# Kernel optimization log

Measured on AMD Instinct MI355X. Metric: run time of the kernel, lower is better.

Reference implementation:

```python
import jax, jax.numpy as jnp
import numpy as np

F = 32          # conf['num_features']
G = 96          # voxel grid extent
N_VOX = 80000   # occupied input voxels
BN_EPS = 1e-5


def _encode(c):
    c = c.astype(np.int64) + 8
    return (c[:, 0] * 512 + c[:, 1]) * 512 + c[:, 2]


def _offsets(ks, dil):
    r = np.arange(-(ks // 2), ks // 2 + 1) * dil
    return np.stack(np.meshgrid(r, r, r, indexing='ij'), -1).reshape(-1, 3)


def _build_map(in_coords, out_coords, offsets):
    # For each kernel offset k and output voxel j, find input voxel index at
    # out_coords[j] + offsets[k]; sentinel = n_in / n_out when absent.
    n_in, n_out = len(in_coords), len(out_coords)
    keys = _encode(in_coords)
    order = np.argsort(keys).astype(np.int32)
    skeys = keys[order]
    K = len(offsets)
    in_map = np.full((K, n_out), n_in, np.int32)
    out_map = np.full((K, n_out), n_out, np.int32)
    base = np.arange(n_out, dtype=np.int32)
    for k, off in enumerate(offsets):
        q = _encode(out_coords + off)
        pos = np.clip(np.searchsorted(skeys, q), 0, n_in - 1)
        valid = skeys[pos] == q
        in_map[k] = np.where(valid, order[pos], n_in)
        out_map[k] = np.where(valid, base, n_out)
    return jnp.asarray(in_map), jnp.asarray(out_map)


def setup_inputs() -> dict:
    rng = np.random.default_rng(0)
    idx = rng.choice(G ** 3, size=N_VOX, replace=False)
    coords = np.stack(np.unravel_index(idx, (G, G, G)), 1).astype(np.int64)
    c2 = np.unique(coords // 2 * 2, axis=0)   # stride-2 coords (enc1 output)
    c4 = np.unique(coords // 4 * 4, axis=0)   # stride-4 coords (c_out.C)

    m1_in, m1_out = _build_map(coords, c2, _offsets(5, 1))  # k5 s2 conv
    m2_in, m2_out = _build_map(c2, c2, _offsets(3, 2))      # enc1 blocks
    m3_in, m3_out = _build_map(c2, c4, _offsets(3, 2))      # conv2 -> c_out.C
    m4_in, m4_out = _build_map(c4, c4, _offsets(3, 4))      # enc2 blocks

    key = jax.random.key(0)
    ks = jax.random.split(key, 8)
    s = 0.05
    return {
        'x_geo': jax.random.normal(ks[0], (N_VOX, 1), jnp.float32),
        'x_col': jax.random.uniform(ks[1], (N_VOX, 3), jnp.float32),
        'w0': jax.random.normal(ks[2], (125, 4, F), jnp.float32) * s,
        'w_e1': jax.random.normal(ks[3], (2, 2, 27, F, F), jnp.float32) * s,
        'g_e1': jnp.ones((2, 2, F), jnp.float32),
        'b_e1': jnp.zeros((2, 2, F), jnp.float32),
        'w2': jax.random.normal(ks[4], (27, F, 2 * F), jnp.float32) * s,
        'w_e2': jax.random.normal(ks[5], (2, 2, 27, 2 * F, 2 * F), jnp.float32) * s,
        'g_e2': jnp.ones((2, 2, 2 * F), jnp.float32),
        'b_e2': jnp.zeros((2, 2, 2 * F), jnp.float32),
        'm1_in': m1_in, 'm1_out': m1_out,
        'm2_in': m2_in, 'm2_out': m2_out,
        'm3_in': m3_in, 'm3_out': m3_out,
        'm4_in': m4_in, 'm4_out': m4_out,
    }


def sparse_conv(feats, W, in_map, out_map):
    # gather -> GEMM -> scatter per kernel offset (lax.scan over K offsets)
    n_out = out_map.shape[1]
    fpad = jnp.concatenate([feats, jnp.zeros((1, feats.shape[1]), feats.dtype)], 0)
    out0 = jnp.zeros((n_out + 1, W.shape[2]), feats.dtype)
    def step(acc, kmw):
        im, om, w = kmw
        return acc.at[om].add(fpad[im] @ w), None
    out, _ = jax.lax.scan(step, out0, (in_map, out_map, W))
    return out[:n_out]


def batch_norm(x, g, b):
    mu = x.mean(0)
    var = ((x - mu) ** 2).mean(0)
    return (x - mu) * jax.lax.rsqrt(var + BN_EPS) * g + b


def basic_block(x, w, g, b, in_map, out_map):
    # ME BasicBlock: conv-BN-ReLU-conv-BN + residual, ReLU
    y = jax.nn.relu(batch_norm(sparse_conv(x, w[0], in_map, out_map), g[0], b[0]))
    y = batch_norm(sparse_conv(y, w[1], in_map, out_map), g[1], b[1])
    return jax.nn.relu(y + x)


def reference(x_geo, x_col, w0, w_e1, g_e1, b_e1, w2, w_e2, g_e2, b_e2,
              m1_in, m1_out, m2_in, m2_out, m3_in, m3_out, m4_in, m4_out):
    x = jnp.concatenate([x_geo, x_col], axis=1)          # ME.cat -> 4 channels
    x = jax.nn.relu(sparse_conv(x, w0, m1_in, m1_out))   # k5 s2 conv + ReLU
    for i in range(2):                                   # enc1 residual blocks
        x = basic_block(x, w_e1[i], g_e1[i], b_e1[i], m2_in, m2_out)
    x = sparse_conv(x, w2, m3_in, m3_out)                # conv2 onto c_out.C
    for i in range(2):                                   # enc2 residual blocks
        x = basic_block(x, w_e2[i], g_e2[i], b_e2[i], m4_in, m4_out)
    return x
```

## Files before the change

kernel.cpp:

```cpp
#include <hip/hip_runtime.h>
#include <hip/hip_bf16.h>


typedef float f4 __attribute__((ext_vector_type(4)));
typedef short short8 __attribute__((ext_vector_type(8)));
typedef short short4v __attribute__((ext_vector_type(4)));

#define BN_EPS 1e-5f

static inline int ceil_div(int a, int b) { return (a + b - 1) / b; }

static __device__ inline float btof(short s) {
    unsigned u = ((unsigned)(unsigned short)s) << 16;
    float f;
    __builtin_memcpy(&f, &u, 4);
    return f;
}
static __device__ inline short ftob(float f) {
    __hip_bfloat16 h = __float2bfloat16(f);
    short s;
    __builtin_memcpy(&s, &h, 2);
    return s;
}

struct Seg {
    const float* W;
    long long begin, end;
    int K, CIN, COUT;
};
struct ProArgs {
    Seg s[10];
    const float* geo;
    const float* col;
    __hip_bfloat16* x0;
    int n_vox;
    float* stats;
    __hip_bfloat16* pads[5];
    int padn[5];
    long long wf_total;
    __hip_bfloat16* Wf;
};

__global__ __launch_bounds__(256) void prologue(ProArgs pa, long long total) {
    long long e = (long long)blockIdx.x * 256 + threadIdx.x;
    if (e >= total) return;
    if (e < pa.wf_total) {
        int si = 0;
#pragma unroll
        for (int i = 0; i < 10; ++i)
            if (e >= pa.s[i].end) si = i + 1;
        const Seg sg = pa.s[si];
        long long r = e - sg.begin;
        int j = (int)(r & 7);
        int lane = (int)((r >> 3) & 63);
        long long rest = r >> 9;
        int NT = sg.COUT >> 4;
        int ntile = (int)(rest % NT);
        int chunk = (int)(rest / NT);
        int kd = chunk * 32 + ((lane >> 4) << 3) + j;
        int koff = kd / sg.CIN;
        int ci = kd % sg.CIN;
        int n = ntile * 16 + (lane & 15);
        float v = (koff < sg.K) ? sg.W[((size_t)koff * sg.CIN + ci) * sg.COUT + n] : 0.f;
        pa.Wf[e] = __float2bfloat16(v);
        return;
    }
    long long r = e - pa.wf_total;
    if (r < pa.n_vox) {
        int row = (int)r;
        pa.x0[row * 4 + 0] = __float2bfloat16(pa.geo[row]);
        pa.x0[row * 4 + 1] = __float2bfloat16(pa.col[row * 3 + 0]);
        pa.x0[row * 4 + 2] = __float2bfloat16(pa.col[row * 3 + 1]);
        pa.x0[row * 4 + 3] = __float2bfloat16(pa.col[row * 3 + 2]);
        return;
    }
    r -= pa.n_vox;
    if (r < 4096) {
        pa.stats[r] = 0.f;
        return;
    }
    r -= 4096;
#pragma unroll
    for (int i = 0; i < 5; ++i) {
        if (r < pa.padn[i]) {
            pa.pads[i][r] = __float2bfloat16(0.f);
            return;
        }
        r -= pa.padn[i];
    }
}

template <int CIN, int COUT, int MT, int K>
__global__ __launch_bounds__(256) void conv_splitk(
    const __hip_bfloat16* __restrict__ feat,
    const __hip_bfloat16* __restrict__ Wf,
    const int* __restrict__ in_map,
    __hip_bfloat16* __restrict__ out,
    float* __restrict__ stats,
    int n_out, int n_in) {
    constexpr int NT = COUT / 16;
    constexpr int H = CIN / 32;
    constexpr int R = MT * 16;
    constexpr int KPW = (K + 3) / 4;
    const int t = threadIdx.x, w = t >> 6, lane = t & 63;
    const int quad = lane >> 4, ml = lane & 15;
    const int mb = blockIdx.x * R;

    __shared__ float red[4][R][COUT];
    __shared__ float sred[2][256];

    f4 acc[MT * NT];
#pragma unroll
    for (int i = 0; i < MT * NT; ++i) acc[i] = (f4){0.f, 0.f, 0.f, 0.f};

    for (int kk = 0; kk < KPW; ++kk) {
        const int k = kk * 4 + w;
        if (k < K) {
            const int* mk = in_map + (size_t)k * n_out;
            int idx[MT];
#pragma unroll
            for (int mi = 0; mi < MT; ++mi) {
                int m = mb + mi * 16 + ml;
                idx[mi] = (m < n_out) ? mk[m] : n_in;
            }
            short8 bfrag[H * NT];
#pragma unroll
            for (int h = 0; h < H; ++h)
#pragma unroll
                for (int nt = 0; nt < NT; ++nt)
                    bfrag[h * NT + nt] = *(const short8*)(
                        Wf + (((size_t)(k * H + h) * NT + nt) * 64 + lane) * 8);
#pragma unroll
            for (int mi = 0; mi < MT; ++mi) {
                const __hip_bfloat16* fp = feat + (size_t)idx[mi] * CIN + quad * 8;
#pragma unroll
                for (int h = 0; h < H; ++h) {
                    short8 a = *(const short8*)(fp + h * 32);
#pragma unroll
                    for (int nt = 0; nt < NT; ++nt)
                        acc[mi * NT + nt] = __builtin_amdgcn_mfma_f32_16x16x32_bf16(
                            a, bfrag[h * NT + nt], acc[mi * NT + nt], 0, 0, 0);
                }
            }
        }
    }

#pragma unroll
    for (int mi = 0; mi < MT; ++mi)
#pragma unroll
        for (int nt = 0; nt < NT; ++nt)
#pragma unroll
            for (int i = 0; i < 4; ++i)
                red[w][mi * 16 + quad * 4 + i][nt * 16 + ml] = acc[mi * NT + nt][i];
    __syncthreads();

    constexpr int E = (R * COUT) / 256;
    constexpr int RSTEP = 256 / COUT;
    const int col = t % COUT;
    const int rg = t / COUT;
    float s = 0.f, s2 = 0.f;
#pragma unroll
    for (int i = 0; i < E; ++i) {
        int r = rg + i * RSTEP;
        float v = red[0][r][col] + red[1][r][col] + red[2][r][col] + red[3][r][col];
        s += v;
        s2 += v * v;
        int grow = mb + r;
        if (grow < n_out) out[(size_t)grow * COUT + col] = __float2bfloat16(v);
    }

    if (stats) {
        sred[0][t] = s;
        sred[1][t] = s2;
        __syncthreads();
        if (t < 2 * COUT) {
            int c = t % COUT;
            int which = t / COUT;
            float v = 0.f;
#pragma unroll
            for (int j = 0; j < RSTEP; ++j) v += sred[which][j * COUT + c];
            atomicAdd(&stats[((blockIdx.x & 3) * 2 + which) * COUT + c], v);
        }
    }
}

__global__ __launch_bounds__(256) void stem_mfma(
    const __hip_bfloat16* __restrict__ feat,
    const __hip_bfloat16* __restrict__ Wf,
    const int* __restrict__ in_map,
    __hip_bfloat16* __restrict__ out,
    int n_out, int n_in) {
    const int t = threadIdx.x, w = t >> 6, lane = t & 63;
    const int quad = lane >> 4, ml = lane & 15;
    const int ntile = w & 1, mgroup = w >> 1;
    const int mb = blockIdx.x * 64 + mgroup * 32;
    const int m0 = mb + ml, m1 = mb + 16 + ml;
    const bool v0 = m0 < n_out, v1 = m1 < n_out;

    f4 acc0 = {0.f, 0.f, 0.f, 0.f};
    f4 acc1 = {0.f, 0.f, 0.f, 0.f};

#pragma unroll 4
    for (int chunk = 0; chunk < 16; ++chunk) {
        int k0 = chunk * 8 + quad * 2;
        int k1 = k0 + 1;
        short8 b = *(const short8*)(Wf + ((size_t)(chunk * 2 + ntile) * 64 + lane) * 8);
        int ia = (v0 && k0 < 125) ? in_map[(size_t)k0 * n_out + m0] : n_in;
        int ib = (v0 && k1 < 125) ? in_map[(size_t)k1 * n_out + m0] : n_in;
        int ic = (v1 && k0 < 125) ? in_map[(size_t)k0 * n_out + m1] : n_in;
        int id = (v1 && k1 < 125) ? in_map[(size_t)k1 * n_out + m1] : n_in;
        short4v pa = *(const short4v*)(feat + (size_t)ia * 4);
        short4v pb = *(const short4v*)(feat + (size_t)ib * 4);
        short4v pc = *(const short4v*)(feat + (size_t)ic * 4);
        short4v pd = *(const short4v*)(feat + (size_t)id * 4);
        short8 a0, a1;
        a0[0] = pa[0]; a0[1] = pa[1]; a0[2] = pa[2]; a0[3] = pa[3];
        a0[4] = pb[0]; a0[5] = pb[1]; a0[6] = pb[2]; a0[7] = pb[3];
        a1[0] = pc[0]; a1[1] = pc[1]; a1[2] = pc[2]; a1[3] = pc[3];
        a1[4] = pd[0]; a1[5] = pd[1]; a1[6] = pd[2]; a1[7] = pd[3];
        acc0 = __builtin_amdgcn_mfma_f32_16x16x32_bf16(a0, b, acc0, 0, 0, 0);
        acc1 = __builtin_amdgcn_mfma_f32_16x16x32_bf16(a1, b, acc1, 0, 0, 0);
    }

    const int col = ntile * 16 + ml;
#pragma unroll
    for (int i = 0; i < 4; ++i) {
        int r0 = mb + quad * 4 + i;
        if (r0 < n_out)
            out[(size_t)r0 * 32 + col] = __float2bfloat16(fmaxf(acc0[i], 0.f));
        int r1 = mb + 16 + quad * 4 + i;
        if (r1 < n_out)
            out[(size_t)r1 * 32 + col] = __float2bfloat16(fmaxf(acc1[i], 0.f));
    }
}

template <int C>
__device__ inline void bn_coef(const float* st, const float* g, const float* b,
                               int c, int n, float& sc, float& sh) {
    float rn = 1.f / (float)n;
    float sum = st[c] + st[2 * C + c] + st[4 * C + c] + st[6 * C + c];
    float sq  = st[C + c] + st[3 * C + c] + st[5 * C + c] + st[7 * C + c];
    float mu = sum * rn;
    float inv = rsqrtf(sq * rn - mu * mu + BN_EPS);
    sc = inv * g[c];
    sh = b[c] - mu * sc;
}

template <int C>
__global__ __launch_bounds__(256) void bn_relu8(
    __hip_bfloat16* __restrict__ x, const float* __restrict__ st,
    const float* __restrict__ g, const float* __restrict__ b, int n) {
    __shared__ float sc[C], sh[C];
    const int t = threadIdx.x;
    if (t < C) bn_coef<C>(st, g, b, t, n, sc[t], sh[t]);
    __syncthreads();
    long long i = (long long)blockIdx.x * 256 + t;
    long long tot = (long long)n * (C / 8);
    if (i >= tot) return;
    int c0 = (int)(i % (C / 8)) * 8;
    short8 v = *(const short8*)(x + i * 8);
    short8 o;
#pragma unroll
    for (int j = 0; j < 8; ++j) {
        float f = btof(v[j]) * sc[c0 + j] + sh[c0 + j];
        o[j] = ftob(fmaxf(f, 0.f));
    }
    *(short8*)(x + i * 8) = o;
}

template <int C>
__global__ __launch_bounds__(256) void bn_res8_bf16(
    const __hip_bfloat16* __restrict__ y, const __hip_bfloat16* __restrict__ res,
    const float* __restrict__ st, const float* __restrict__ g,
    const float* __restrict__ b, __hip_bfloat16* __restrict__ out, int n) {
    __shared__ float sc[C], sh[C];
    const int t = threadIdx.x;
    if (t < C) bn_coef<C>(st, g, b, t, n, sc[t], sh[t]);
    __syncthreads();
    long long i = (long long)blockIdx.x * 256 + t;
    long long tot = (long long)n * (C / 8);
    if (i >= tot) return;
    int c0 = (int)(i % (C / 8)) * 8;
    short8 v = *(const short8*)(y + i * 8);
    short8 r = *(const short8*)(res + i * 8);
    short8 o;
#pragma unroll
    for (int j = 0; j < 8; ++j) {
        float f = btof(v[j]) * sc[c0 + j] + sh[c0 + j] + btof(r[j]);
        o[j] = ftob(fmaxf(f, 0.f));
    }
    *(short8*)(out + i * 8) = o;
}

template <int C>
__global__ __launch_bounds__(256) void bn_res8_f32(
    const __hip_bfloat16* __restrict__ y, const __hip_bfloat16* __restrict__ res,
    const float* __restrict__ st, const float* __restrict__ g,
    const float* __restrict__ b, float* __restrict__ out, int n) {
    __shared__ float sc[C], sh[C];
    const int t = threadIdx.x;
    if (t < C) bn_coef<C>(st, g, b, t, n, sc[t], sh[t]);
    __syncthreads();
    long long i = (long long)blockIdx.x * 256 + t;
    long long tot = (long long)n * (C / 8);
    if (i >= tot) return;
    int c0 = (int)(i % (C / 8)) * 8;
    short8 v = *(const short8*)(y + i * 8);
    short8 r = *(const short8*)(res + i * 8);
    f4 o0, o1;
#pragma unroll
    for (int j = 0; j < 8; ++j) {
        float f = btof(v[j]) * sc[c0 + j] + sh[c0 + j] + btof(r[j]);
        f = fmaxf(f, 0.f);
        if (j < 4) o0[j] = f; else o1[j - 4] = f;
    }
    *(f4*)(out + i * 8) = o0;
    *(f4*)(out + i * 8 + 4) = o1;
}

extern "C" void kernel_launch(void* const* d_in, const int* in_sizes, int n_in_cnt,
                              void* d_out, int out_size, void* d_ws, size_t ws_size,
                              hipStream_t stream) {
    const float* x_geo = (const float*)d_in[0];
    const float* x_col = (const float*)d_in[1];
    const float* w0    = (const float*)d_in[2];
    const float* w_e1  = (const float*)d_in[3];
    const float* g_e1  = (const float*)d_in[4];
    const float* b_e1  = (const float*)d_in[5];
    const float* w2    = (const float*)d_in[6];
    const float* w_e2  = (const float*)d_in[7];
    const float* g_e2  = (const float*)d_in[8];
    const float* b_e2  = (const float*)d_in[9];
    const int* m1_in = (const int*)d_in[10];
    const int* m2_in = (const int*)d_in[12];
    const int* m3_in = (const int*)d_in[14];
    const int* m4_in = (const int*)d_in[16];

    const int n_vox = in_sizes[0];
    const int nc2 = in_sizes[10] / 125;
    const int nc4 = in_sizes[14] / 27;
    (void)out_size; (void)ws_size; (void)n_in_cnt;

    char* p = (char*)d_ws;
    auto alloc = [&](size_t bytes) -> char* {
        char* r = p;
        p += (bytes + 255) & ~(size_t)255;
        return r;
    };
    float* stats = (float*)alloc(8 * 512 * sizeof(float));
    __hip_bfloat16* x0 = (__hip_bfloat16*)alloc((size_t)(n_vox + 1) * 4 * 2);
    __hip_bfloat16* A  = (__hip_bfloat16*)alloc((size_t)(nc2 + 1) * 32 * 2);
    __hip_bfloat16* B  = (__hip_bfloat16*)alloc((size_t)(nc2 + 1) * 32 * 2);
    __hip_bfloat16* Cb = (__hip_bfloat16*)alloc((size_t)(nc2 + 1) * 32 * 2);
    __hip_bfloat16* D  = (__hip_bfloat16*)alloc((size_t)(nc4 + 1) * 64 * 2);
    __hip_bfloat16* E  = (__hip_bfloat16*)alloc((size_t)(nc4 + 1) * 64 * 2);
    __hip_bfloat16* Fb = (__hip_bfloat16*)alloc((size_t)(nc4 + 1) * 64 * 2);

    const long long sz_stem = 16LL * 2 * 512;
    const long long sz_e1   = 27LL * 2 * 512;
    const long long sz_c2   = 27LL * 4 * 512;
    const long long sz_e2   = 54LL * 4 * 512;
    const long long wf_total = sz_stem + 4 * sz_e1 + sz_c2 + 4 * sz_e2;
    __hip_bfloat16* Wf = (__hip_bfloat16*)alloc((size_t)wf_total * 2);

    long long off_stem = 0;
    long long off_e1[4], off_e2[4];
    long long cur = sz_stem;
    for (int i = 0; i < 4; ++i) { off_e1[i] = cur; cur += sz_e1; }
    long long off_c2 = cur; cur += sz_c2;
    for (int i = 0; i < 4; ++i) { off_e2[i] = cur; cur += sz_e2; }

    ProArgs pa;
    cur = 0;
    auto seg = [&](int i, const float* W, int K, int CIN, int COUT, long long n) {
        pa.s[i].W = W; pa.s[i].K = K; pa.s[i].CIN = CIN; pa.s[i].COUT = COUT;
        pa.s[i].begin = cur; pa.s[i].end = cur + n; cur += n;
    };
    seg(0, w0, 125, 4, 32, sz_stem);
    for (int i = 0; i < 4; ++i)
        seg(1 + i, w_e1 + (size_t)i * 27 * 32 * 32, 27, 32, 32, sz_e1);
    seg(5, w2, 27, 32, 64, sz_c2);
    for (int i = 0; i < 4; ++i)
        seg(6 + i, w_e2 + (size_t)i * 27 * 64 * 64, 27, 64, 64, sz_e2);
    pa.geo = x_geo; pa.col = x_col; pa.x0 = x0; pa.n_vox = n_vox;
    pa.stats = stats;
    pa.pads[0] = x0 + (size_t)n_vox * 4; pa.padn[0] = 4;
    pa.pads[1] = A + (size_t)nc2 * 32;   pa.padn[1] = 32;
    pa.pads[2] = B + (size_t)nc2 * 32;   pa.padn[2] = 32;
    pa.pads[3] = D + (size_t)nc4 * 64;   pa.padn[3] = 64;
    pa.pads[4] = E + (size_t)nc4 * 64;   pa.padn[4] = 64;
    pa.wf_total = wf_total;
    pa.Wf = Wf;
    long long pro_total = wf_total + n_vox + 4096 + (4 + 32 + 32 + 64 + 64);
    prologue<<<ceil_div((int)pro_total, 256), 256, 0, stream>>>(pa, pro_total);

    stem_mfma<<<ceil_div(nc2, 64), 256, 0, stream>>>(x0, Wf + off_stem, m1_in, A,
                                                     nc2, n_vox);

    int slot = 0;
    for (int blk = 0; blk < 2; ++blk) {
        const float* gA = g_e1 + (blk * 2 + 0) * 32, *bA = b_e1 + (blk * 2 + 0) * 32;
        const float* gB = g_e1 + (blk * 2 + 1) * 32, *bB = b_e1 + (blk * 2 + 1) * 32;
        conv_splitk<32, 32, 2, 27><<<ceil_div(nc2, 32), 256, 0, stream>>>(
            A, Wf + off_e1[blk * 2 + 0], m2_in, B, stats + slot * 512, nc2, nc2);
        bn_relu8<32><<<ceil_div(nc2 * 4, 256), 256, 0, stream>>>(
            B, stats + slot * 512, gA, bA, nc2);
        ++slot;
        conv_splitk<32, 32, 2, 27><<<ceil_div(nc2, 32), 256, 0, stream>>>(
            B, Wf + off_e1[blk * 2 + 1], m2_in, Cb, stats + slot * 512, nc2, nc2);
        bn_res8_bf16<32><<<ceil_div(nc2 * 4, 256), 256, 0, stream>>>(
            Cb, A, stats + slot * 512, gB, bB, A, nc2);
        ++slot;
    }

    conv_splitk<32, 64, 1, 27><<<ceil_div(nc4, 16), 256, 0, stream>>>(
        A, Wf + off_c2, m3_in, D, nullptr, nc4, nc2);

    for (int blk = 0; blk < 2; ++blk) {
        const float* gA = g_e2 + (blk * 2 + 0) * 64, *bA = b_e2 + (blk * 2 + 0) * 64;
        const float* gB = g_e2 + (blk * 2 + 1) * 64, *bB = b_e2 + (blk * 2 + 1) * 64;
        conv_splitk<64, 64, 1, 27><<<ceil_div(nc4, 16), 256, 0, stream>>>(
            D, Wf + off_e2[blk * 2 + 0], m4_in, E, stats + slot * 512, nc4, nc4);
        bn_relu8<64><<<ceil_div(nc4 * 8, 256), 256, 0, stream>>>(
            E, stats + slot * 512, gA, bA, nc4);
        ++slot;
        conv_splitk<64, 64, 1, 27><<<ceil_div(nc4, 16), 256, 0, stream>>>(
            E, Wf + off_e2[blk * 2 + 1], m4_in, Fb, stats + slot * 512, nc4, nc4);
        if (blk == 0) {
            bn_res8_bf16<64><<<ceil_div(nc4 * 8, 256), 256, 0, stream>>>(
                Fb, D, stats + slot * 512, gB, bB, D, nc4);
        } else {
            bn_res8_f32<64><<<ceil_div(nc4 * 8, 256), 256, 0, stream>>>(
                Fb, D, stats + slot * 512, gB, bB, (float*)d_out, nc4);
        }
        ++slot;
    }
}
```

Before: 360.1 us.

## Fuse BN+ReLU of first block conv into second conv's gather

Drops the standalone bn_relu8 kernels. The second conv of each residual block now applies batch-norm scale/shift and ReLU to the gathered bf16 features as it loads them, masking sentinel rows to zero. The K loop is fully unrolled with a clamped map row, so out-of-range kernel offsets read weights from an extra zero-padded slot (weight buffers are sized up by one offset) instead of branching. This saves a launch and a full read/write pass per block. In exchange, the normalization arithmetic is repeated for every gathered neighbour (up to 27 times per voxel) and register pressure rises.

```diff
diff --git a/kernel.cpp b/kernel.cpp
--- a/kernel.cpp
+++ b/kernel.cpp
@@ -90,13 +90,28 @@
     }
 }
 
-template <int CIN, int COUT, int MT, int K>
+template <int C>
+__device__ inline void bn_coef(const float* st, const float* g, const float* b,
+                               int c, int n, float& sc, float& sh) {
+    float rn = 1.f / (float)n;
+    float sum = st[c] + st[2 * C + c] + st[4 * C + c] + st[6 * C + c];
+    float sq  = st[C + c] + st[3 * C + c] + st[5 * C + c] + st[7 * C + c];
+    float mu = sum * rn;
+    float inv = rsqrtf(sq * rn - mu * mu + BN_EPS);
+    sc = inv * g[c];
+    sh = b[c] - mu * sc;
+}
+
+template <int CIN, int COUT, int MT, int K, bool BNF>
 __global__ __launch_bounds__(256) void conv_splitk(
     const __hip_bfloat16* __restrict__ feat,
     const __hip_bfloat16* __restrict__ Wf,
     const int* __restrict__ in_map,
     __hip_bfloat16* __restrict__ out,
     float* __restrict__ stats,
+    const float* __restrict__ in_stats,
+    const float* __restrict__ in_g,
+    const float* __restrict__ in_b,
     int n_out, int n_in) {
     constexpr int NT = COUT / 16;
     constexpr int H = CIN / 32;
@@ -108,39 +123,70 @@
 
     __shared__ float red[4][R][COUT];
     __shared__ float sred[2][256];
+    __shared__ float isc[CIN], ish[CIN];
+
+    if (BNF) {
+        if (t < CIN) {
+            float sc, sh;
+            bn_coef<CIN>(in_stats, in_g, in_b, t, n_in, sc, sh);
+            isc[t] = sc;
+            ish[t] = sh;
+        }
+        __syncthreads();
+    }
+    float scr[H][8], shr[H][8];
+    if (BNF) {
+#pragma unroll
+        for (int h = 0; h < H; ++h)
+#pragma unroll
+            for (int j = 0; j < 8; ++j) {
+                int ch = h * 32 + quad * 8 + j;
+                scr[h][j] = isc[ch];
+                shr[h][j] = ish[ch];
+            }
+    }
 
     f4 acc[MT * NT];
 #pragma unroll
     for (int i = 0; i < MT * NT; ++i) acc[i] = (f4){0.f, 0.f, 0.f, 0.f};
 
+#pragma unroll
     for (int kk = 0; kk < KPW; ++kk) {
         const int k = kk * 4 + w;
-        if (k < K) {
-            const int* mk = in_map + (size_t)k * n_out;
-            int idx[MT];
-#pragma unroll
-            for (int mi = 0; mi < MT; ++mi) {
-                int m = mb + mi * 16 + ml;
-                idx[mi] = (m < n_out) ? mk[m] : n_in;
-            }
-            short8 bfrag[H * NT];
-#pragma unroll
-            for (int h = 0; h < H; ++h)
+        const int krow = (k < K) ? k : 0;
+        const int* mk = in_map + (size_t)krow * n_out;
+        int idx[MT];
+#pragma unroll
+        for (int mi = 0; mi < MT; ++mi) {
+            int m = mb + mi * 16 + ml;
+            idx[mi] = (m < n_out) ? mk[m] : n_in;
+        }
+        short8 bfrag[H * NT];
+#pragma unroll
+        for (int h = 0; h < H; ++h)
+#pragma unroll
+            for (int nt = 0; nt < NT; ++nt)
+                bfrag[h * NT + nt] = *(const short8*)(
+                    Wf + (((size_t)(k * H + h) * NT + nt) * 64 + lane) * 8);
+#pragma unroll
+        for (int mi = 0; mi < MT; ++mi) {
+            const __hip_bfloat16* fp = feat + (size_t)idx[mi] * CIN + quad * 8;
+            const bool sent = (idx[mi] == n_in);
+#pragma unroll
+            for (int h = 0; h < H; ++h) {
+                short8 a = *(const short8*)(fp + h * 32);
+                if (BNF) {
+#pragma unroll
+                    for (int j = 0; j < 8; ++j) {
+                        float f = btof(a[j]) * scr[h][j] + shr[h][j];
+                        f = fmaxf(f, 0.f);
+                        a[j] = sent ? (short)0 : ftob(f);
+                    }
+                }
 #pragma unroll
                 for (int nt = 0; nt < NT; ++nt)
-                    bfrag[h * NT + nt] = *(const short8*)(
-                        Wf + (((size_t)(k * H + h) * NT + nt) * 64 + lane) * 8);
-#pragma unroll
-            for (int mi = 0; mi < MT; ++mi) {
-                const __hip_bfloat16* fp = feat + (size_t)idx[mi] * CIN + quad * 8;
-#pragma unroll
-                for (int h = 0; h < H; ++h) {
-                    short8 a = *(const short8*)(fp + h * 32);
-#pragma unroll
-                    for (int nt = 0; nt < NT; ++nt)
-                        acc[mi * NT + nt] = __builtin_amdgcn_mfma_f32_16x16x32_bf16(
-                            a, bfrag[h * NT + nt], acc[mi * NT + nt], 0, 0, 0);
-                }
+                    acc[mi * NT + nt] = __builtin_amdgcn_mfma_f32_16x16x32_bf16(
+                        a, bfrag[h * NT + nt], acc[mi * NT + nt], 0, 0, 0);
             }
         }
     }
@@ -204,11 +250,13 @@
     for (int chunk = 0; chunk < 16; ++chunk) {
         int k0 = chunk * 8 + quad * 2;
         int k1 = k0 + 1;
+        int k0c = (k0 < 125) ? k0 : 0;
+        int k1c = (k1 < 125) ? k1 : 0;
         short8 b = *(const short8*)(Wf + ((size_t)(chunk * 2 + ntile) * 64 + lane) * 8);
-        int ia = (v0 && k0 < 125) ? in_map[(size_t)k0 * n_out + m0] : n_in;
-        int ib = (v0 && k1 < 125) ? in_map[(size_t)k1 * n_out + m0] : n_in;
-        int ic = (v1 && k0 < 125) ? in_map[(size_t)k0 * n_out + m1] : n_in;
-        int id = (v1 && k1 < 125) ? in_map[(size_t)k1 * n_out + m1] : n_in;
+        int ia = v0 ? in_map[(size_t)k0c * n_out + m0] : n_in;
+        int ib = v0 ? in_map[(size_t)k1c * n_out + m0] : n_in;
+        int ic = v1 ? in_map[(size_t)k0c * n_out + m1] : n_in;
+        int id = v1 ? in_map[(size_t)k1c * n_out + m1] : n_in;
         short4v pa = *(const short4v*)(feat + (size_t)ia * 4);
         short4v pb = *(const short4v*)(feat + (size_t)ib * 4);
         short4v pc = *(const short4v*)(feat + (size_t)ic * 4);
@@ -232,40 +280,6 @@
         if (r1 < n_out)
             out[(size_t)r1 * 32 + col] = __float2bfloat16(fmaxf(acc1[i], 0.f));
     }
-}
-
-template <int C>
-__device__ inline void bn_coef(const float* st, const float* g, const float* b,
-                               int c, int n, float& sc, float& sh) {
-    float rn = 1.f / (float)n;
-    float sum = st[c] + st[2 * C + c] + st[4 * C + c] + st[6 * C + c];
-    float sq  = st[C + c] + st[3 * C + c] + st[5 * C + c] + st[7 * C + c];
-    float mu = sum * rn;
-    float inv = rsqrtf(sq * rn - mu * mu + BN_EPS);
-    sc = inv * g[c];
-    sh = b[c] - mu * sc;
-}
-
-template <int C>
-__global__ __launch_bounds__(256) void bn_relu8(
-    __hip_bfloat16* __restrict__ x, const float* __restrict__ st,
-    const float* __restrict__ g, const float* __restrict__ b, int n) {
-    __shared__ float sc[C], sh[C];
-    const int t = threadIdx.x;
-    if (t < C) bn_coef<C>(st, g, b, t, n, sc[t], sh[t]);
-    __syncthreads();
-    long long i = (long long)blockIdx.x * 256 + t;
-    long long tot = (long long)n * (C / 8);
-    if (i >= tot) return;
-    int c0 = (int)(i % (C / 8)) * 8;
-    short8 v = *(const short8*)(x + i * 8);
-    short8 o;
-#pragma unroll
-    for (int j = 0; j < 8; ++j) {
-        float f = btof(v[j]) * sc[c0 + j] + sh[c0 + j];
-        o[j] = ftob(fmaxf(f, 0.f));
-    }
-    *(short8*)(x + i * 8) = o;
 }
 
 template <int C>
@@ -357,9 +371,9 @@
     __hip_bfloat16* Fb = (__hip_bfloat16*)alloc((size_t)(nc4 + 1) * 64 * 2);
 
     const long long sz_stem = 16LL * 2 * 512;
-    const long long sz_e1   = 27LL * 2 * 512;
-    const long long sz_c2   = 27LL * 4 * 512;
-    const long long sz_e2   = 54LL * 4 * 512;
+    const long long sz_e1   = 28LL * 2 * 512;
+    const long long sz_c2   = 28LL * 4 * 512;
+    const long long sz_e2   = 56LL * 4 * 512;
     const long long wf_total = sz_stem + 4 * sz_e1 + sz_c2 + 4 * sz_e2;
     __hip_bfloat16* Wf = (__hip_bfloat16*)alloc((size_t)wf_total * 2);
 
@@ -401,38 +415,37 @@
     for (int blk = 0; blk < 2; ++blk) {
         const float* gA = g_e1 + (blk * 2 + 0) * 32, *bA = b_e1 + (blk * 2 + 0) * 32;
         const float* gB = g_e1 + (blk * 2 + 1) * 32, *bB = b_e1 + (blk * 2 + 1) * 32;
-        conv_splitk<32, 32, 2, 27><<<ceil_div(nc2, 32), 256, 0, stream>>>(
-            A, Wf + off_e1[blk * 2 + 0], m2_in, B, stats + slot * 512, nc2, nc2);
-        bn_relu8<32><<<ceil_div(nc2 * 4, 256), 256, 0, stream>>>(
-            B, stats + slot * 512, gA, bA, nc2);
-        ++slot;
-        conv_splitk<32, 32, 2, 27><<<ceil_div(nc2, 32), 256, 0, stream>>>(
-            B, Wf + off_e1[blk * 2 + 1], m2_in, Cb, stats + slot * 512, nc2, nc2);
+        conv_splitk<32, 32, 2, 27, false><<<ceil_div(nc2, 32), 256, 0, stream>>>(
+            A, Wf + off_e1[blk * 2 + 0], m2_in, B, stats + slot * 512,
+            nullptr, nullptr, nullptr, nc2, nc2);
+        conv_splitk<32, 32, 2, 27, true><<<ceil_div(nc2, 32), 256, 0, stream>>>(
+            B, Wf + off_e1[blk * 2 + 1], m2_in, Cb, stats + (slot + 1) * 512,
+            stats + slot * 512, gA, bA, nc2, nc2);
         bn_res8_bf16<32><<<ceil_div(nc2 * 4, 256), 256, 0, stream>>>(
-            Cb, A, stats + slot * 512, gB, bB, A, nc2);
-        ++slot;
-    }
-
-    conv_splitk<32, 64, 1, 27><<<ceil_div(nc4, 16), 256, 0, stream>>>(
-        A, Wf + off_c2, m3_in, D, nullptr, nc4, nc2);
+            Cb, A, stats + (slot + 1) * 512, gB, bB, A, nc2);
+        slot += 2;
+    }
+
+    conv_splitk<32, 64, 1, 27, false><<<ceil_div(nc4, 16), 256, 0, stream>>>(
+        A, Wf + off_c2, m3_in, D, nullptr,
+        nullptr, nullptr, nullptr, nc4, nc2);
 
     for (int blk = 0; blk < 2; ++blk) {
         const float* gA = g_e2 + (blk * 2 + 0) * 64, *bA = b_e2 + (blk * 2 + 0) * 64;
         const float* gB = g_e2 + (blk * 2 + 1) * 64, *bB = b_e2 + (blk * 2 + 1) * 64;
-        conv_splitk<64, 64, 1, 27><<<ceil_div(nc4, 16), 256, 0, stream>>>(
-            D, Wf + off_e2[blk * 2 + 0], m4_in, E, stats + slot * 512, nc4, nc4);
-        bn_relu8<64><<<ceil_div(nc4 * 8, 256), 256, 0, stream>>>(
-            E, stats + slot * 512, gA, bA, nc4);
-        ++slot;
-        conv_splitk<64, 64, 1, 27><<<ceil_div(nc4, 16), 256, 0, stream>>>(
-            E, Wf + off_e2[blk * 2 + 1], m4_in, Fb, stats + slot * 512, nc4, nc4);
+        conv_splitk<64, 64, 1, 27, false><<<ceil_div(nc4, 16), 256, 0, stream>>>(
+            D, Wf + off_e2[blk * 2 + 0], m4_in, E, stats + slot * 512,
+            nullptr, nullptr, nullptr, nc4, nc4);
+        conv_splitk<64, 64, 1, 27, true><<<ceil_div(nc4, 16), 256, 0, stream>>>(
+            E, Wf + off_e2[blk * 2 + 1], m4_in, Fb, stats + (slot + 1) * 512,
+            stats + slot * 512, gA, bA, nc4, nc4);
         if (blk == 0) {
             bn_res8_bf16<64><<<ceil_div(nc4 * 8, 256), 256, 0, stream>>>(
-                Fb, D, stats + slot * 512, gB, bB, D, nc4);
+                Fb, D, stats + (slot + 1) * 512, gB, bB, D, nc4);
         } else {
             bn_res8_f32<64><<<ceil_div(nc4 * 8, 256), 256, 0, stream>>>(
-                Fb, D, stats + slot * 512, gB, bB, (float*)d_out, nc4);
-        }
-        ++slot;
-    }
-}
+                Fb, D, stats + (slot + 1) * 512, gB, bB, (float*)d_out, nc4);
+        }
+        slot += 2;
+    }
+}
```

Measured after the change: 341.6 us. 1.05x faster.
